# Kernel optimization log

Measured on AMD Instinct MI355X. Metric: run time of the kernel, lower is better.

## Reference

```python
import jax, jax.numpy as jnp
import numpy as np

B = 8
NUM_CLASSES = 80
STRIDES = (8, 16, 32, 64, 128)
HS = (96, 48, 24, 12, 6)
WS = (160, 80, 40, 20, 10)
IMG_H, IMG_W = 768, 1280
OCTAVE_SCALE = 4.0
LOC_THR = 0.01
SCORE_THR = 0.05
IOU_THR = 0.5
NMS_PRE = 1000
MAX_PER_IMG = 100
MAX_RATIO_ANCHOR = abs(float(np.log(1e-6)))        # anchor_coder wh_ratio_clip=1e-6
MAX_RATIO_BBOX = abs(float(np.log(16.0 / 1000.0)))  # bbox_coder default wh_ratio_clip
CLS_OFFSET = 4096.0  # > max image coord, separates classes for class-aware NMS


def setup_inputs():
    inp = {}
    k = 0
    for i, (h, w) in enumerate(zip(HS, WS)):
        for name, c in (("cls_score", NUM_CLASSES), ("bbox_pred", 4), ("shape_pred", 2), ("loc_pred", 1)):
            k += 1
            inp[f"{name}_{i}"] = jax.random.normal(jax.random.fold_in(jax.random.key(0), k), (B, c, h, w), dtype=jnp.float32)
    return inp


def _squares(h, w, stride):
    # mmdet square anchor generator: base size stride*octave_base_scale, ratio 1, center offset 0
    xs = jnp.arange(w, dtype=jnp.float32) * stride
    ys = jnp.arange(h, dtype=jnp.float32) * stride
    yy, xx = jnp.meshgrid(ys, xs, indexing="ij")
    half = 0.5 * OCTAVE_SCALE * stride
    return jnp.stack([xx - half, yy - half, xx + half, yy + half], -1).reshape(-1, 4)


def _delta2bbox(rois, deltas, max_ratio, max_shape=None):
    dx, dy = deltas[..., 0], deltas[..., 1]
    dw = jnp.clip(deltas[..., 2], -max_ratio, max_ratio)
    dh = jnp.clip(deltas[..., 3], -max_ratio, max_ratio)
    px = (rois[..., 0] + rois[..., 2]) * 0.5
    py = (rois[..., 1] + rois[..., 3]) * 0.5
    pw = rois[..., 2] - rois[..., 0]
    ph = rois[..., 3] - rois[..., 1]
    gx = px + pw * dx
    gy = py + ph * dy
    gw = pw * jnp.exp(dw)
    gh = ph * jnp.exp(dh)
    x1, y1 = gx - 0.5 * gw, gy - 0.5 * gh
    x2, y2 = gx + 0.5 * gw, gy + 0.5 * gh
    if max_shape is not None:
        x1 = jnp.clip(x1, 0.0, float(max_shape[1]))
        x2 = jnp.clip(x2, 0.0, float(max_shape[1]))
        y1 = jnp.clip(y1, 0.0, float(max_shape[0]))
        y2 = jnp.clip(y2, 0.0, float(max_shape[0]))
    return jnp.stack([x1, y1, x2, y2], -1)


def _level(cls, bbox, shp, loc, stride, h, w):
    b = cls.shape[0]
    # NOTE: double sigmoid is faithful to the original wrapper (it sigmoids twice)
    scores = jax.nn.sigmoid(jax.nn.sigmoid(jnp.transpose(cls, (0, 2, 3, 1)).reshape(b, -1, NUM_CLASSES)))
    mask = (jax.nn.sigmoid(loc) >= LOC_THR).astype(scores.dtype)
    mask = jnp.transpose(mask, (0, 2, 3, 1)).reshape(b, -1)  # num_anchors == 1
    scores = scores * mask[:, :, None]
    deltas = jnp.transpose(shp, (0, 2, 3, 1)).reshape(b, -1, 2)
    bdel = jnp.concatenate([jnp.zeros_like(deltas), deltas], axis=-1)  # [0,0,dw,dh]
    anchors = _delta2bbox(_squares(h, w, stride)[None], bdel, MAX_RATIO_ANCHOR)  # guided anchors
    bbox = jnp.transpose(bbox, (0, 2, 3, 1)).reshape(b, -1, 4)
    n = scores.shape[1]
    if n < NMS_PRE:  # pad_with_value
        pad = NMS_PRE - n
        scores = jnp.pad(scores, ((0, 0), (0, pad), (0, 0)))
        bbox = jnp.pad(bbox, ((0, 0), (0, pad), (0, 0)))
        anchors = jnp.pad(anchors, ((0, 0), (0, pad), (0, 0)))
    _, idx = jax.lax.top_k(scores.max(-1), NMS_PRE)
    scores = jnp.take_along_axis(scores, idx[:, :, None], axis=1)
    bbox = jnp.take_along_axis(bbox, idx[:, :, None], axis=1)
    anchors = jnp.take_along_axis(anchors, idx[:, :, None], axis=1)
    proposals = _delta2bbox(anchors, bbox, MAX_RATIO_BBOX, (IMG_H, IMG_W))
    return scores, proposals


def _iou_one_vs_all(box, boxes):
    lt = jnp.maximum(box[:2], boxes[:, :2])
    rb = jnp.minimum(box[2:], boxes[:, 2:])
    wh = jnp.clip(rb - lt, 0.0, None)
    inter = wh[:, 0] * wh[:, 1]
    a1 = (box[2] - box[0]) * (box[3] - box[1])
    a2 = (boxes[:, 2] - boxes[:, 0]) * (boxes[:, 3] - boxes[:, 1])
    return inter / (a1 + a2 - inter + 1e-6)


def _nms_single(scores, boxes):
    # class-aware greedy NMS (BatchedNMS semantics): scores [N,C], boxes [N,4]
    n, c = scores.shape
    s = jnp.where(scores > SCORE_THR, scores, 0.0).reshape(-1)  # [N*C]
    offs = (jnp.arange(c, dtype=boxes.dtype) * CLS_OFFSET)[None, :, None]
    cboxes = (boxes[:, None, :] + offs).reshape(-1, 4)  # class-offset boxes

    def step(sv, _):
        i = jnp.argmax(sv)
        sc = sv[i]
        keep = sc > 0.0
        iou = _iou_one_vs_all(cboxes[i], cboxes)
        sv = jnp.where(iou > IOU_THR, 0.0, sv)  # suppresses i itself too
        cls = jnp.where(keep, (i % c).astype(jnp.int32), -1)
        return sv, (boxes[i // c], sc, cls, keep)

    _, (ob, osc, ocls, okeep) = jax.lax.scan(step, s, None, length=MAX_PER_IMG)
    kf = okeep.astype(boxes.dtype)
    return okeep.sum().astype(jnp.int32), ob * kf[:, None], osc * kf, ocls


def _forward(tensors):
    mlvl_scores, mlvl_props = [], []
    for i in range(5):
        s, p = _level(tensors[4 * i], tensors[4 * i + 1], tensors[4 * i + 2], tensors[4 * i + 3],
                      STRIDES[i], HS[i], WS[i])
        mlvl_scores.append(s)
        mlvl_props.append(p)
    scores = jnp.concatenate(mlvl_scores, axis=1)   # [B, 5000, 80]
    props = jnp.concatenate(mlvl_props, axis=1)     # [B, 5000, 4]
    k = min(max(1000, NMS_PRE), scores.shape[1])
    _, idx = jax.lax.top_k(scores.max(-1), k)
    scores = jnp.take_along_axis(scores, idx[:, :, None], axis=1)
    props = jnp.take_along_axis(props, idx[:, :, None], axis=1)
    return jax.vmap(_nms_single)(scores, props)


def reference(cls_score_0, bbox_pred_0, shape_pred_0, loc_pred_0,
              cls_score_1, bbox_pred_1, shape_pred_1, loc_pred_1,
              cls_score_2, bbox_pred_2, shape_pred_2, loc_pred_2,
              cls_score_3, bbox_pred_3, shape_pred_3, loc_pred_3,
              cls_score_4, bbox_pred_4, shape_pred_4, loc_pred_4):
    tensors = [cls_score_0, bbox_pred_0, shape_pred_0, loc_pred_0,
               cls_score_1, bbox_pred_1, shape_pred_1, loc_pred_1,
               cls_score_2, bbox_pred_2, shape_pred_2, loc_pred_2,
               cls_score_3, bbox_pred_3, shape_pred_3, loc_pred_3,
               cls_score_4, bbox_pred_4, shape_pred_4, loc_pred_4]
    num_detected, proposals, out_scores, cls_id = _forward(tensors)
    return num_detected, proposals, out_scores, cls_id
```

## Files before the change

kernel.cpp:

```cpp
#include <hip/hip_runtime.h>
#include <stdint.h>

#define NCLS 80
#define BATCH 8
#define NA 20460
#define TOPK 1000
#define MAXPER 100
#define CAP 8
#define POOL 256
#define IMG_WF 1280.0f
#define IMG_HF 768.0f
#define CLS_OFF 4096.0f
#define MAX_RATIO_ANCHOR 13.815510557964274f
#define MAX_RATIO_BBOX   4.1351665567423557f

#define K2_HALF_UP (0.5 + 0x1p-25)

__constant__ int   c_lvoff[6]  = {0, 15360, 19200, 20160, 20400, 20460};
__constant__ int   c_lvoff4[6] = {0, 3840, 4800, 5040, 5100, 5115};
__constant__ int   c_lw[5]    = {160, 80, 40, 20, 10};
__constant__ int   c_lh[5]    = {96, 48, 24, 12, 6};
__constant__ float c_ls[5]    = {8.f, 16.f, 32.f, 64.f, 128.f};

struct InPtrs {
  const float* cls[5];
  const float* bbox[5];
  const float* shp[5];
  const float* loc[5];
};

__device__ __forceinline__ float sigf(float x) { return 1.0f / (1.0f + expf(-x)); }

__device__ __forceinline__ int wave_red_sum_i32(int v) {
  int t;
  t = __builtin_amdgcn_update_dpp(0, v, 0x111, 0xf, 0xf, false); v += t;
  t = __builtin_amdgcn_update_dpp(0, v, 0x112, 0xf, 0xf, false); v += t;
  t = __builtin_amdgcn_update_dpp(0, v, 0x114, 0xf, 0xf, false); v += t;
  t = __builtin_amdgcn_update_dpp(0, v, 0x118, 0xf, 0xf, false); v += t;
  t = __builtin_amdgcn_update_dpp(0, v, 0x142, 0xf, 0xf, false); v += t;
  t = __builtin_amdgcn_update_dpp(0, v, 0x143, 0xf, 0xf, false); v += t;
  return __builtin_amdgcn_readlane(v, 63);
}
__device__ __forceinline__ void wave_red_top2(unsigned m1, unsigned m2,
                                              unsigned& r1, unsigned& r2) {
#define T2STEP(ctrl) { \
    unsigned o1 = (unsigned)__builtin_amdgcn_update_dpp(0, (int)m1, ctrl, 0xf, 0xf, false); \
    unsigned o2 = (unsigned)__builtin_amdgcn_update_dpp(0, (int)m2, ctrl, 0xf, 0xf, false); \
    unsigned tm = min(m1, o1); \
    m1 = max(m1, o1); \
    m2 = max(tm, max(m2, o2)); }
  T2STEP(0x111) T2STEP(0x112) T2STEP(0x114) T2STEP(0x118) T2STEP(0x142) T2STEP(0x143)
#undef T2STEP
  r1 = (unsigned)__builtin_amdgcn_readlane((int)m1, 63);
  r2 = (unsigned)__builtin_amdgcn_readlane((int)m2, 63);
}

__global__ __launch_bounds__(256) void k_maxscore(InPtrs P, float* maxscore) {
  int gid = blockIdx.x * 256 + threadIdx.x;
  int p = gid >> 2;
  int h = gid & 3;
  if (p >= BATCH * (NA / 4)) return;
  int b = p / (NA / 4);
  int q = p - b * (NA / 4);
  int l = 0;
  while (q >= c_lvoff4[l + 1]) ++l;
  int hw = c_lh[l] * c_lw[l];
  int sp = (q - c_lvoff4[l]) * 4;
  const float4* cls = (const float4*)(P.cls[l] + (size_t)(b * NCLS + h * 20) * hw + sp);
  int s4 = hw >> 2;
  float4 m = cls[0];
  for (int c = 1; c < NCLS / 4; ++c) {
    float4 v = cls[(size_t)c * s4];
    m.x = fmaxf(m.x, v.x); m.y = fmaxf(m.y, v.y);
    m.z = fmaxf(m.z, v.z); m.w = fmaxf(m.w, v.w);
  }
  #pragma unroll
  for (int o = 1; o < 4; o <<= 1) {
    m.x = fmaxf(m.x, __shfl_xor(m.x, o, 64));
    m.y = fmaxf(m.y, __shfl_xor(m.y, o, 64));
    m.z = fmaxf(m.z, __shfl_xor(m.z, o, 64));
    m.w = fmaxf(m.w, __shfl_xor(m.w, o, 64));
  }
  if (h == 0) {
    float4 lo = *(const float4*)(P.loc[l] + (size_t)b * hw + sp);
    float4 r;
    r.x = (sigf(lo.x) >= 0.01f) ? sigf(sigf(m.x)) : 0.0f;
    r.y = (sigf(lo.y) >= 0.01f) ? sigf(sigf(m.y)) : 0.0f;
    r.z = (sigf(lo.z) >= 0.01f) ? sigf(sigf(m.z)) : 0.0f;
    r.w = (sigf(lo.w) >= 0.01f) ? sigf(sigf(m.w)) : 0.0f;
    ((float4*)maxscore)[(size_t)b * (NA / 4) + q] = r;
  }
}

__global__ __launch_bounds__(1024) void k_select(const float* maxscore, int* sel) {
  int b = blockIdx.x;
  const unsigned int* ms = (const unsigned int*)(maxscore + (size_t)b * NA);
  int tid = threadIdx.x;
  int wv = tid >> 6;
  int lane = tid & 63;
  __shared__ unsigned s_h[2048];
  __shared__ int s_wtot[16];
  __shared__ int s_res[2];
  __shared__ unsigned long long s_A[1024];
  __shared__ unsigned long long s_B[1024];

  unsigned w[20];
  #pragma unroll
  for (int k = 0; k < 5; ++k) {
    int q = tid * 5 + k;
    uint4 u = (q < NA / 4) ? ((const uint4*)ms)[q] : make_uint4(0u, 0u, 0u, 0u);
    w[k * 4 + 0] = u.x & 0x3FFFFFu;
    w[k * 4 + 1] = u.y & 0x3FFFFFu;
    w[k * 4 + 2] = u.z & 0x3FFFFFu;
    w[k * 4 + 3] = u.w & 0x3FFFFFu;
  }
  int lim = NA - tid * 20;
  lim = (lim < 0) ? 0 : ((lim > 20) ? 20 : lim);

  s_h[tid] = 0u; s_h[tid + 1024] = 0u;
  __syncthreads();

  auto scanFind = [&](int target) {
    int b0 = 2047 - 2 * tid;
    int h0 = (int)s_h[b0];
    int h1 = (int)s_h[b0 - 1];
    int pair = h0 + h1;
    int incl = pair;
    #pragma unroll
    for (int o = 1; o < 64; o <<= 1) {
      int uu = __shfl_up(incl, o, 64);
      if (lane >= o) incl += uu;
    }
    if (lane == 63) s_wtot[wv] = incl;
    __syncthreads();
    int woff = 0;
    #pragma unroll
    for (int ww = 0; ww < 16; ++ww) woff += (ww < wv) ? s_wtot[ww] : 0;
    int excl = woff + incl - pair;
    if (excl < target && excl + h0 >= target) { s_res[0] = b0; s_res[1] = excl; }
    int e1 = excl + h0;
    if (e1 < target && e1 + h1 >= target) { s_res[0] = b0 - 1; s_res[1] = e1; }
    __syncthreads();
  };

  #pragma unroll
  for (int k = 0; k < 20; ++k) atomicAdd(&s_h[w[k] >> 11], 1u);
  __syncthreads();
  scanFind(TOPK);
  int B1 = s_res[0];
  int NGT1 = s_res[1];

  s_h[tid] = 0u; s_h[tid + 1024] = 0u;
  __syncthreads();
  #pragma unroll
  for (int k = 0; k < 20; ++k)
    if ((int)(w[k] >> 11) == B1) atomicAdd(&s_h[w[k] & 0x7FFu], 1u);
  __syncthreads();
  scanFind(TOPK - NGT1);
  unsigned V = ((unsigned)B1 << 11) | (unsigned)s_res[0];

  if (tid < 1024 - TOPK) s_A[TOPK + tid] = 0ull;

  int cgt = 0;
  #pragma unroll
  for (int k = 0; k < 20; ++k) cgt += (w[k] > V) ? 1 : 0;
  {
    int incl = cgt;
    #pragma unroll
    for (int o = 1; o < 64; o <<= 1) {
      int uu = __shfl_up(incl, o, 64);
      if (lane >= o) incl += uu;
    }
    if (lane == 63) s_wtot[wv] = incl;
    __syncthreads();
    int woff = 0, tot = 0;
    #pragma unroll
    for (int ww = 0; ww < 16; ++ww) { tot += s_wtot[ww]; woff += (ww < wv) ? s_wtot[ww] : 0; }
    int pos = woff + incl - cgt;
    #pragma unroll
    for (int k = 0; k < 20; ++k) {
      if (w[k] > V) {
        int i = tid * 20 + k;
        s_A[pos++] = ((unsigned long long)w[k] << 32) |
                     (unsigned long long)(0xFFFFFFFFu - (unsigned)i);
      }
    }
    int ngt = tot;
    int need = TOPK - ngt;
    __syncthreads();

    int ceq = 0;
    #pragma unroll
    for (int k = 0; k < 20; ++k) if (k < lim && w[k] == V) ++ceq;
    int incl2 = ceq;
    #pragma unroll
    for (int o = 1; o < 64; o <<= 1) {
      int uu = __shfl_up(incl2, o, 64);
      if (lane >= o) incl2 += uu;
    }
    if (lane == 63) s_wtot[wv] = incl2;
    __syncthreads();
    int woff2 = 0;
    #pragma unroll
    for (int ww = 0; ww < 16; ++ww) woff2 += (ww < wv) ? s_wtot[ww] : 0;
    int r = woff2 + incl2 - ceq;
    #pragma unroll
    for (int k = 0; k < 20; ++k) {
      if (k < lim && w[k] == V) {
        if (r < need) {
          int i = tid * 20 + k;
          s_A[ngt + r] = ((unsigned long long)V << 32) |
                         (unsigned long long)(0xFFFFFFFFu - (unsigned)i);
        }
        ++r;
      }
    }
  }
  __syncthreads();

  unsigned long long key = s_A[tid];
  int tog = 0;
  for (unsigned k = 2; k <= 1024; k <<= 1) {
    for (unsigned j = k >> 1; j > 0; j >>= 1) {
      unsigned long long other;
      if (j >= 64) {
        unsigned long long* cur = tog ? s_A : s_B;
        cur[tid] = key;
        __syncthreads();
        other = cur[tid ^ (int)j];
        tog ^= 1;
      } else {
        other = __shfl_xor(key, (int)j, 64);
      }
      bool takeMax = (((tid & (int)k) == 0) == ((tid & (int)j) == 0));
      unsigned long long mx = (key > other) ? key : other;
      unsigned long long mn = (key > other) ? other : key;
      key = takeMax ? mx : mn;
    }
  }
  if (tid < TOPK) {
    sel[b * TOPK + tid] = (int)(0xFFFFFFFFu - (unsigned)(key & 0xFFFFFFFFull));
  }
}

__global__ __launch_bounds__(256) void k_gather(InPtrs P, const int* sel, float* boxes, float* sv) {
  int wvi = threadIdx.x >> 6;
  int lane = threadIdx.x & 63;
  int wid = blockIdx.x * 4 + wvi;
  int b = wid / TOPK;
  int r = wid - b * TOPK;
  __shared__ float s_sc[4][NCLS];

  int a = sel[b * TOPK + r];
  int l = 0;
  while (a >= c_lvoff[l + 1]) ++l;
  int within = a - c_lvoff[l];
  int W = c_lw[l], H = c_lh[l];
  int y = within / W, x = within - y * W;
  int hw = H * W;
  int sp = within;
  float stride = c_ls[l];
  float px = (float)x * stride;
  float py = (float)y * stride;
  float pw = 4.0f * stride;

  const float* shp = P.shp[l];
  float dws = shp[(b * 2 + 0) * hw + sp];
  float dhs = shp[(b * 2 + 1) * hw + sp];
  dws = fminf(fmaxf(dws, -MAX_RATIO_ANCHOR), MAX_RATIO_ANCHOR);
  dhs = fminf(fmaxf(dhs, -MAX_RATIO_ANCHOR), MAX_RATIO_ANCHOR);
  float gw = pw * expf(dws);
  float gh = pw * expf(dhs);
  float ax1 = px - 0.5f * gw, ax2 = px + 0.5f * gw;
  float ay1 = py - 0.5f * gh, ay2 = py + 0.5f * gh;

  const float* bb = P.bbox[l];
  float dx = bb[(b * 4 + 0) * hw + sp];
  float dy = bb[(b * 4 + 1) * hw + sp];
  float dw = bb[(b * 4 + 2) * hw + sp];
  float dh = bb[(b * 4 + 3) * hw + sp];
  dw = fminf(fmaxf(dw, -MAX_RATIO_BBOX), MAX_RATIO_BBOX);
  dh = fminf(fmaxf(dh, -MAX_RATIO_BBOX), MAX_RATIO_BBOX);
  float px2 = (ax1 + ax2) * 0.5f, py2 = (ay1 + ay2) * 0.5f;
  float pw2 = ax2 - ax1, ph2 = ay2 - ay1;
  float gx = px2 + pw2 * dx, gy = py2 + ph2 * dy;
  float gw2 = pw2 * expf(dw), gh2 = ph2 * expf(dh);
  float x1 = fminf(fmaxf(gx - 0.5f * gw2, 0.0f), IMG_WF);
  float x2 = fminf(fmaxf(gx + 0.5f * gw2, 0.0f), IMG_WF);
  float y1 = fminf(fmaxf(gy - 0.5f * gh2, 0.0f), IMG_HF);
  float y2 = fminf(fmaxf(gy + 0.5f * gh2, 0.0f), IMG_HF);
  if (lane == 0) {
    float4 st; st.x = x1; st.y = y1; st.z = x2; st.w = y2;
    ((float4*)boxes)[b * TOPK + r] = st;
  }

  const float* cls = P.cls[l];
  float sl = sigf(P.loc[l][b * hw + sp]);
  bool mask = (sl >= 0.01f);
  int base = (b * NCLS) * hw + sp;
  for (int c = lane; c < NCLS; c += 64) {
    float vv = 0.0f;
    if (mask) {
      float s2 = sigf(sigf(cls[base + c * hw]));
      vv = (s2 > 0.05f) ? s2 : 0.0f;
    }
    s_sc[wvi][c] = vv;
  }
  __syncthreads();
  int t = threadIdx.x;
  if (t < NCLS) {
    int r0 = blockIdx.x * 4 - b * TOPK;
    float4 o; o.x = s_sc[0][t]; o.y = s_sc[1][t]; o.z = s_sc[2][t]; o.w = s_sc[3][t];
    *(float4*)(sv + ((size_t)(b * NCLS + t) * TOPK + r0)) = o;
  }
}

__global__ __launch_bounds__(256) void k_nms(const float* boxes, const float* sv,
                                             float* keptScore, int* keptRow, int* kc,
                                             const int* flags, const int* gbits, int cap) {
  int bc = blockIdx.x;
  if (flags && flags[bc] == 0) return;
  int b = bc / NCLS;
  int c = bc - b * NCLS;
  int tid = threadIdx.x;
  int wv = tid >> 6, lane = tid & 63;

  unsigned Glow = 0u;
  if (gbits) Glow = ((unsigned)gbits[b]) & 0x3FFFFFu;

  __shared__ float4 s_box[TOPK];
  __shared__ float  s_ard[TOPK];
  __shared__ unsigned long long s_p2[2][4];

  float x1[4], y1[4], x2[4], y2[4], ar[4];
  unsigned key[4];
  float off = (float)c * CLS_OFF;
  const float* svc = sv + (size_t)(b * NCLS + c) * TOPK;
  #pragma unroll
  for (int j = 0; j < 4; ++j) {
    int row = j * 256 + tid;
    if (row < TOPK) {
      float4 bo = ((const float4*)boxes)[b * TOPK + row];
      float a = bo.x + off, d = bo.y + off, e = bo.z + off, f = bo.w + off;
      x1[j] = a; y1[j] = d; x2[j] = e; y2[j] = f;
      ar[j] = (e - a) * (f - d);
      unsigned bits = __float_as_uint(svc[row]);
      key[j] = ((bits & 0x3FFFFFu) << 10) | (1023u - (unsigned)row);
      float sden = ar[j] + 1e-6f;
      bool deg = !((double)ar[j] > (double)sden * K2_HALF_UP);
      float4 sb; sb.x = a; sb.y = d; sb.z = e; sb.w = f;
      s_box[row] = sb;
      s_ard[row] = __uint_as_float(__float_as_uint(ar[j]) | (deg ? 0x80000000u : 0u));
    } else {
      x1[j] = y1[j] = x2[j] = y2[j] = ar[j] = 0.0f;
      key[j] = 0u;
    }
  }
  __syncthreads();

  int kept = 0;
  bool sticky = false;
  float* ks = keptScore + (size_t)(b * NCLS + c) * MAXPER;
  int*   kr = keptRow   + (size_t)(b * NCLS + c) * MAXPER;

  for (int round = 0; round < cap; ++round) {
    int par = round & 1;
    unsigned hi1 = max(key[0], key[1]), lo1 = min(key[0], key[1]);
    unsigned hi2 = max(key[2], key[3]), lo2 = min(key[2], key[3]);
    unsigned m1 = max(hi1, hi2);
    unsigned m2 = max(min(hi1, hi2), max(lo1, lo2));
    unsigned w1, w2;
    wave_red_top2(m1, m2, w1, w2);
    if (lane == 0) s_p2[par][wv] = ((unsigned long long)w1 << 32) | w2;
    __syncthreads();
    unsigned k0 = 0u, k1 = 0u;
    #pragma unroll
    for (int w = 0; w < 4; ++w) {
      unsigned long long pp = s_p2[par][w];
      unsigned p1 = (unsigned)(pp >> 32), p2 = (unsigned)pp;
      unsigned tm = min(k0, p1);
      k0 = max(k0, p1);
      k1 = max(tm, max(k1, p2));
    }
    if (k0 < 1024u) break;
    if ((k0 >> 10) < Glow) break;
    int brow1 = 1023 - (int)(k0 & 1023u);
    float bs1 = __uint_as_float(0x3F000000u | (k0 >> 10));
    float4 bb1 = s_box[brow1];
    unsigned au1 = __float_as_uint(s_ard[brow1]);
    bool deg1 = (au1 >> 31) != 0u;
    float ba1 = __uint_as_float(au1 & 0x7FFFFFFFu);
    if (tid == 0) { ks[kept] = bs1; kr[kept] = brow1; }
    kept++;
    if (deg1) { sticky = true; break; }
    if (kept >= cap) break;
    bool live2 = (k1 >= 1024u) && ((k1 >> 10) >= Glow);
    if (!live2) break;
    bool do2 = false, deg2 = false;
    float4 bb2; float ba2 = 0.0f;
    {
      int brow2 = 1023 - (int)(k1 & 1023u);
      float bs2 = __uint_as_float(0x3F000000u | (k1 >> 10));
      bb2 = s_box[brow2];
      unsigned au2 = __float_as_uint(s_ard[brow2]);
      deg2 = (au2 >> 31) != 0u;
      ba2 = __uint_as_float(au2 & 0x7FFFFFFFu);
      float ltx = fmaxf(bb1.x, bb2.x), rbx = fminf(bb1.z, bb2.z);
      float lty = fmaxf(bb1.y, bb2.y), rby = fminf(bb1.w, bb2.w);
      float w_ = fmaxf(rbx - ltx, 0.0f), h_ = fmaxf(rby - lty, 0.0f);
      float inter = w_ * h_;
      float denom = ((ba1 + ba2) - inter) + 1e-6f;
      if (!((double)inter > (double)denom * K2_HALF_UP)) {
        do2 = true;
        if (tid == 0) { ks[kept] = bs2; kr[kept] = brow2; }
        kept++;
      }
    }
    if (do2 && deg2) { sticky = true; break; }
    #pragma unroll
    for (int j = 0; j < 4; ++j) {
      {
        float ltx = fmaxf(bb1.x, x1[j]), rbx = fminf(bb1.z, x2[j]);
        float lty = fmaxf(bb1.y, y1[j]), rby = fminf(bb1.w, y2[j]);
        float w_ = fmaxf(rbx - ltx, 0.0f), h_ = fmaxf(rby - lty, 0.0f);
        float inter = w_ * h_;
        float denom = ((ba1 + ar[j]) - inter) + 1e-6f;
        if ((double)inter > (double)denom * K2_HALF_UP) key[j] = 0u;
      }
      if (do2) {
        float ltx = fmaxf(bb2.x, x1[j]), rbx = fminf(bb2.z, x2[j]);
        float lty = fmaxf(bb2.y, y1[j]), rby = fminf(bb2.w, y2[j]);
        float w_ = fmaxf(rbx - ltx, 0.0f), h_ = fmaxf(rby - lty, 0.0f);
        float inter = w_ * h_;
        float denom = ((ba2 + ar[j]) - inter) + 1e-6f;
        if ((double)inter > (double)denom * K2_HALF_UP) key[j] = 0u;
      }
    }
    if (kept >= cap) break;
  }
  if (tid == 0) kc[b * NCLS + c] = sticky ? -kept : kept;
}

__global__ __launch_bounds__(256) void k_cut(const float* keptScore, const int* kc,
                                             int* flags, int* gbits) {
  int b = blockIdx.x;
  int tid = threadIdx.x;
  int wv = tid >> 6, lane = tid & 63;
  __shared__ int s_abs[NCLS];
  __shared__ int s_neg[NCLS];
  __shared__ unsigned s_h[2048];
  __shared__ int s_wtot[4];
  __shared__ int s_res[2];
  __shared__ int s_tot[4];

  if (tid < NCLS) {
    int v = kc[b * NCLS + tid];
    s_abs[tid] = (v < 0) ? -v : v;
    s_neg[tid] = (v < 0) ? 1 : 0;
  }
  #pragma unroll
  for (int j = 0; j < 8; ++j) s_h[tid * 8 + j] = 0u;
  __syncthreads();

  unsigned vv[3] = {0u, 0u, 0u};
  #pragma unroll
  for (int t = 0; t < 3; ++t) {
    int e = tid + t * 256;
    if (e < NCLS * CAP) {
      int c = e / CAP, k = e - c * CAP;
      if (k < s_abs[c])
        vv[t] = __float_as_uint(keptScore[(size_t)b * NCLS * MAXPER + c * MAXPER + k])
                & 0x3FFFFFu;
    }
  }
  int live = ((vv[0] != 0u) ? 1 : 0) + ((vv[1] != 0u) ? 1 : 0) + ((vv[2] != 0u) ? 1 : 0);
  live = wave_red_sum_i32(live);
  if (lane == 0) s_tot[wv] = live;
  #pragma unroll
  for (int t = 0; t < 3; ++t) if (vv[t]) atomicAdd(&s_h[vv[t] >> 11], 1u);
  __syncthreads();
  int T = s_tot[0] + s_tot[1] + s_tot[2] + s_tot[3];

  auto scanFind = [&](int target) {
    int base = 2047 - 8 * tid;
    int h[8]; int loc = 0;
    #pragma unroll
    for (int j = 0; j < 8; ++j) { h[j] = (int)s_h[base - j]; loc += h[j]; }
    int incl = loc;
    #pragma unroll
    for (int o = 1; o < 64; o <<= 1) {
      int uu = __shfl_up(incl, o, 64);
      if (lane >= o) incl += uu;
    }
    if (lane == 63) s_wtot[wv] = incl;
    __syncthreads();
    int woff = 0;
    #pragma unroll
    for (int ww = 0; ww < 4; ++ww) woff += (ww < wv) ? s_wtot[ww] : 0;
    int e = woff + incl - loc;
    #pragma unroll
    for (int j = 0; j < 8; ++j) {
      if (e < target && e + h[j] >= target) { s_res[0] = base - j; s_res[1] = e; }
      e += h[j];
    }
    __syncthreads();
  };

  unsigned G = 0u;
  if (T >= MAXPER) {
    scanFind(MAXPER);
    int B1 = s_res[0], NGT1 = s_res[1];
    #pragma unroll
    for (int j = 0; j < 8; ++j) s_h[tid * 8 + j] = 0u;
    __syncthreads();
    #pragma unroll
    for (int t = 0; t < 3; ++t)
      if (vv[t] && (int)(vv[t] >> 11) == B1) atomicAdd(&s_h[vv[t] & 0x7FFu], 1u);
    __syncthreads();
    scanFind(MAXPER - NGT1);
    G = 0x3F000000u | ((unsigned)B1 << 11) | (unsigned)s_res[0];
  }
  if (tid == 0) gbits[b] = (int)G;
  if (tid < NCLS) {
    int f = 0;
    if (s_abs[tid] == CAP && !s_neg[tid]) {
      unsigned slast = __float_as_uint(
          keptScore[(size_t)b * NCLS * MAXPER + tid * MAXPER + (CAP - 1)]);
      if (slast >= G) f = 1;
    }
    flags[b * NCLS + tid] = f;
  }
}

__global__ __launch_bounds__(256) void k_merge(const float* boxes, const float* keptScore,
                                               const int* keptRow, const int* kc, float* out) {
  int b = blockIdx.x;
  int tid = threadIdx.x;
  int wv = tid >> 6, lane = tid & 63;
  __shared__ int s_kc[NCLS];
  __shared__ unsigned s_h[2048];
  __shared__ int s_wtot[4];
  __shared__ int s_res[2];
  __shared__ int s_tot[4];
  __shared__ int s_pos;
  __shared__ int s_sticky;
  __shared__ int s_navail;
  __shared__ unsigned long long s_pool[POOL];
  __shared__ unsigned long long s_sorted[POOL];

  for (int c = tid; c < NCLS; c += 256) s_kc[c] = kc[b * NCLS + c];
  if (tid == 0) { s_pos = 0; s_sticky = 0x7FFFFFFF; s_navail = 0; }
  for (int i = tid; i < POOL; i += 256) { s_pool[i] = 0ull; s_sorted[i] = 0ull; }
  #pragma unroll
  for (int j = 0; j < 8; ++j) s_h[tid * 8 + j] = 0u;
  __syncthreads();

  unsigned sc[32];
  #pragma unroll
  for (int s = 0; s < 32; ++s) {
    int i = tid + s * 256;
    unsigned vvv = 0u;
    if (i < NCLS * MAXPER) {
      int c = i / MAXPER, k = i - c * MAXPER;
      int kcv = s_kc[c];
      int ka = (kcv < 0) ? -kcv : kcv;
      if (k < ka)
        vvv = __float_as_uint(keptScore[(size_t)b * NCLS * MAXPER + i]) & 0x3FFFFFu;
    }
    sc[s] = vvv;
  }
  int live = 0;
  #pragma unroll
  for (int s = 0; s < 32; ++s) live += (sc[s] != 0u) ? 1 : 0;
  live = wave_red_sum_i32(live);
  if (lane == 0) s_tot[wv] = live;
  #pragma unroll
  for (int s = 0; s < 32; ++s) if (sc[s]) atomicAdd(&s_h[sc[s] >> 11], 1u);
  __syncthreads();
  int T = s_tot[0] + s_tot[1] + s_tot[2] + s_tot[3];

  auto scanFind = [&](int target) {
    int base = 2047 - 8 * tid;
    int h[8]; int loc = 0;
    #pragma unroll
    for (int j = 0; j < 8; ++j) { h[j] = (int)s_h[base - j]; loc += h[j]; }
    int incl = loc;
    #pragma unroll
    for (int o = 1; o < 64; o <<= 1) {
      int uu = __shfl_up(incl, o, 64);
      if (lane >= o) incl += uu;
    }
    if (lane == 63) s_wtot[wv] = incl;
    __syncthreads();
    int woff = 0;
    #pragma unroll
    for (int ww = 0; ww < 4; ++ww) woff += (ww < wv) ? s_wtot[ww] : 0;
    int e = woff + incl - loc;
    #pragma unroll
    for (int j = 0; j < 8; ++j) {
      if (e < target && e + h[j] >= target) { s_res[0] = base - j; s_res[1] = e; }
      e += h[j];
    }
    __syncthreads();
  };

  unsigned V = 1u;
  if (T > MAXPER) {
    scanFind(MAXPER);
    int B1 = s_res[0], NGT1 = s_res[1];
    #pragma unroll
    for (int j = 0; j < 8; ++j) s_h[tid * 8 + j] = 0u;
    __syncthreads();
    #pragma unroll
    for (int s = 0; s < 32; ++s)
      if (sc[s] && (int)(sc[s] >> 11) == B1) atomicAdd(&s_h[sc[s] & 0x7FFu], 1u);
    __syncthreads();
    scanFind(MAXPER - NGT1);
    V = ((unsigned)B1 << 11) | (unsigned)s_res[0];
  }

  #pragma unroll
  for (int s = 0; s < 32; ++s) {
    if (sc[s] >= V && sc[s] != 0u) {
      int i = tid + s * 256;
      int c = i / MAXPER, k = i - c * MAXPER;
      int kcv = s_kc[c];
      int ka = (kcv < 0) ? -kcv : kcv;
      unsigned st = (kcv < 0 && k == ka - 1) ? 1u : 0u;
      unsigned row = (unsigned)keptRow[(size_t)b * NCLS * MAXPER + i];
      unsigned flat = row * 80u + (unsigned)c;
      int p = atomicAdd(&s_pos, 1);
      if (p < POOL)
        s_pool[p] = ((unsigned long long)(0x3F000000u | sc[s]) << 32) |
                    (unsigned long long)(0x7FFFFFFFu - ((flat << 1) | st));
    }
  }
  __syncthreads();

  if (tid < POOL) {
    unsigned long long mykey = s_pool[tid];
    if (mykey != 0ull) {
      int rank = 0;
      #pragma unroll 8
      for (int s = 0; s < POOL; ++s) rank += (s_pool[s] > mykey) ? 1 : 0;
      s_sorted[rank] = mykey;
    }
  }
  __syncthreads();

  if (tid < MAXPER) {
    unsigned long long key = s_sorted[tid];
    if (key != 0ull) {
      atomicAdd(&s_navail, 1);
      if ((((unsigned)key) & 1u) == 0u) atomicMin(&s_sticky, tid);
    }
  }
  __syncthreads();
  int navail = s_navail;
  int p = s_sticky;
  int n = (p < navail) ? MAXPER : navail;

  if (tid == 0) out[b] = (float)n;
  const int OB = BATCH;
  const int OP = OB + BATCH * MAXPER * 4;
  const int OS = OP + BATCH * MAXPER;
  if (tid < MAXPER) {
    int k = tid;
    float bx0 = 0.f, bx1 = 0.f, bx2 = 0.f, bx3 = 0.f, scf = 0.f, cf = -1.0f;
    if (k < n) {
      int idx = (k > p) ? p : k;
      unsigned long long key = s_sorted[idx];
      unsigned flat = (0x7FFFFFFFu - (unsigned)key) >> 1;
      unsigned cls = flat % 80u;
      unsigned row = flat / 80u;
      float4 bo = ((const float4*)boxes)[b * TOPK + row];
      bx0 = bo.x; bx1 = bo.y; bx2 = bo.z; bx3 = bo.w;
      scf = __uint_as_float((unsigned)(key >> 32));
      cf = (float)cls;
    }
    float* po = out + OB + (size_t)(b * MAXPER + k) * 4;
    po[0] = bx0; po[1] = bx1; po[2] = bx2; po[3] = bx3;
    out[OP + b * MAXPER + k] = scf;
    out[OS + b * MAXPER + k] = cf;
  }
}

extern "C" void kernel_launch(void* const* d_in, const int* in_sizes, int n_in,
                              void* d_out, int out_size, void* d_ws, size_t ws_size,
                              hipStream_t stream) {
  InPtrs P;
  for (int l = 0; l < 5; ++l) {
    P.cls[l]  = (const float*)d_in[4 * l + 0];
    P.bbox[l] = (const float*)d_in[4 * l + 1];
    P.shp[l]  = (const float*)d_in[4 * l + 2];
    P.loc[l]  = (const float*)d_in[4 * l + 3];
  }
  float* maxscore  = (float*)d_ws;
  int*   sel       = (int*)(maxscore + BATCH * NA);
  float* boxes     = (float*)(sel + BATCH * TOPK);
  float* sv        = boxes + BATCH * TOPK * 4;
  float* keptScore = sv + BATCH * NCLS * TOPK;
  int*   keptRow   = (int*)(keptScore + BATCH * NCLS * MAXPER);
  int*   kc        = keptRow + BATCH * NCLS * MAXPER;
  int*   flags     = kc + BATCH * NCLS;
  int*   gbits     = flags + BATCH * NCLS;
  float* out = (float*)d_out;

  k_maxscore<<<(BATCH * (NA / 4) * 4 + 255) / 256, 256, 0, stream>>>(P, maxscore);
  k_select<<<BATCH, 1024, 0, stream>>>(maxscore, sel);
  k_gather<<<BATCH * TOPK / 4, 256, 0, stream>>>(P, sel, boxes, sv);
  k_nms<<<BATCH * NCLS, 256, 0, stream>>>(boxes, sv, keptScore, keptRow, kc,
                                          (const int*)nullptr, (const int*)nullptr, CAP);
  k_cut<<<BATCH, 256, 0, stream>>>(keptScore, kc, flags, gbits);
  k_nms<<<BATCH * NCLS, 256, 0, stream>>>(boxes, sv, keptScore, keptRow, kc,
                                          flags, gbits, MAXPER);
  k_merge<<<BATCH, 256, 0, stream>>>(boxes, keptScore, keptRow, kc, out);
}
```

Measured before the change: 194.7 us.

## Widen k_merge to 1024 threads and compact the candidate pool with a prefix scan

k_merge now runs 1024 threads per image instead of 256. Each thread holds 8 candidate scores instead of 32, and the histogram scan covers 2 bins per thread across 16 waves. The shared atomic counter that placed survivors into the pool is replaced by a wave and block prefix sum, which gives each thread its write offsets directly. The aim is to cut the latency of this single-block-per-image tail kernel, at the cost of more barriers and cross-wave reductions. Only 8 blocks launch, so any effect on total time is limited.

```diff
diff --git a/kernel.cpp b/kernel.cpp
--- a/kernel.cpp
+++ b/kernel.cpp
@@ -532,33 +532,30 @@
   }
 }
 
-__global__ __launch_bounds__(256) void k_merge(const float* boxes, const float* keptScore,
-                                               const int* keptRow, const int* kc, float* out) {
+__global__ __launch_bounds__(1024) void k_merge(const float* boxes, const float* keptScore,
+                                                const int* keptRow, const int* kc, float* out) {
   int b = blockIdx.x;
   int tid = threadIdx.x;
   int wv = tid >> 6, lane = tid & 63;
   __shared__ int s_kc[NCLS];
   __shared__ unsigned s_h[2048];
-  __shared__ int s_wtot[4];
+  __shared__ int s_wtot[16];
   __shared__ int s_res[2];
-  __shared__ int s_tot[4];
-  __shared__ int s_pos;
   __shared__ int s_sticky;
   __shared__ int s_navail;
   __shared__ unsigned long long s_pool[POOL];
   __shared__ unsigned long long s_sorted[POOL];
 
-  for (int c = tid; c < NCLS; c += 256) s_kc[c] = kc[b * NCLS + c];
-  if (tid == 0) { s_pos = 0; s_sticky = 0x7FFFFFFF; s_navail = 0; }
-  for (int i = tid; i < POOL; i += 256) { s_pool[i] = 0ull; s_sorted[i] = 0ull; }
-  #pragma unroll
-  for (int j = 0; j < 8; ++j) s_h[tid * 8 + j] = 0u;
-  __syncthreads();
-
-  unsigned sc[32];
-  #pragma unroll
-  for (int s = 0; s < 32; ++s) {
-    int i = tid + s * 256;
+  if (tid < NCLS) s_kc[tid] = kc[b * NCLS + tid];
+  if (tid == 0) { s_sticky = 0x7FFFFFFF; s_navail = 0; }
+  if (tid < POOL) { s_pool[tid] = 0ull; s_sorted[tid] = 0ull; }
+  s_h[tid] = 0u; s_h[tid + 1024] = 0u;
+  __syncthreads();
+
+  unsigned sc[8];
+  #pragma unroll
+  for (int s = 0; s < 8; ++s) {
+    int i = tid + s * 1024;
     unsigned vvv = 0u;
     if (i < NCLS * MAXPER) {
       int c = i / MAXPER, k = i - c * MAXPER;
@@ -571,20 +568,22 @@
   }
   int live = 0;
   #pragma unroll
-  for (int s = 0; s < 32; ++s) live += (sc[s] != 0u) ? 1 : 0;
+  for (int s = 0; s < 8; ++s) live += (sc[s] != 0u) ? 1 : 0;
   live = wave_red_sum_i32(live);
-  if (lane == 0) s_tot[wv] = live;
-  #pragma unroll
-  for (int s = 0; s < 32; ++s) if (sc[s]) atomicAdd(&s_h[sc[s] >> 11], 1u);
-  __syncthreads();
-  int T = s_tot[0] + s_tot[1] + s_tot[2] + s_tot[3];
+  if (lane == 0) s_wtot[wv] = live;
+  #pragma unroll
+  for (int s = 0; s < 8; ++s) if (sc[s]) atomicAdd(&s_h[sc[s] >> 11], 1u);
+  __syncthreads();
+  int T = 0;
+  #pragma unroll
+  for (int ww = 0; ww < 16; ++ww) T += s_wtot[ww];
 
   auto scanFind = [&](int target) {
-    int base = 2047 - 8 * tid;
-    int h[8]; int loc = 0;
-    #pragma unroll
-    for (int j = 0; j < 8; ++j) { h[j] = (int)s_h[base - j]; loc += h[j]; }
-    int incl = loc;
+    int b0 = 2047 - 2 * tid;
+    int h0 = (int)s_h[b0];
+    int h1 = (int)s_h[b0 - 1];
+    int pair = h0 + h1;
+    int incl = pair;
     #pragma unroll
     for (int o = 1; o < 64; o <<= 1) {
       int uu = __shfl_up(incl, o, 64);
@@ -594,13 +593,11 @@
     __syncthreads();
     int woff = 0;
     #pragma unroll
-    for (int ww = 0; ww < 4; ++ww) woff += (ww < wv) ? s_wtot[ww] : 0;
-    int e = woff + incl - loc;
-    #pragma unroll
-    for (int j = 0; j < 8; ++j) {
-      if (e < target && e + h[j] >= target) { s_res[0] = base - j; s_res[1] = e; }
-      e += h[j];
-    }
+    for (int ww = 0; ww < 16; ++ww) woff += (ww < wv) ? s_wtot[ww] : 0;
+    int excl = woff + incl - pair;
+    if (excl < target && excl + h0 >= target) { s_res[0] = b0; s_res[1] = excl; }
+    int e1 = excl + h0;
+    if (e1 < target && e1 + h1 >= target) { s_res[0] = b0 - 1; s_res[1] = e1; }
     __syncthreads();
   };
 
@@ -608,31 +605,47 @@
   if (T > MAXPER) {
     scanFind(MAXPER);
     int B1 = s_res[0], NGT1 = s_res[1];
-    #pragma unroll
-    for (int j = 0; j < 8; ++j) s_h[tid * 8 + j] = 0u;
-    __syncthreads();
-    #pragma unroll
-    for (int s = 0; s < 32; ++s)
+    s_h[tid] = 0u; s_h[tid + 1024] = 0u;
+    __syncthreads();
+    #pragma unroll
+    for (int s = 0; s < 8; ++s)
       if (sc[s] && (int)(sc[s] >> 11) == B1) atomicAdd(&s_h[sc[s] & 0x7FFu], 1u);
     __syncthreads();
     scanFind(MAXPER - NGT1);
     V = ((unsigned)B1 << 11) | (unsigned)s_res[0];
   }
 
-  #pragma unroll
-  for (int s = 0; s < 32; ++s) {
-    if (sc[s] >= V && sc[s] != 0u) {
-      int i = tid + s * 256;
-      int c = i / MAXPER, k = i - c * MAXPER;
-      int kcv = s_kc[c];
-      int ka = (kcv < 0) ? -kcv : kcv;
-      unsigned st = (kcv < 0 && k == ka - 1) ? 1u : 0u;
-      unsigned row = (unsigned)keptRow[(size_t)b * NCLS * MAXPER + i];
-      unsigned flat = row * 80u + (unsigned)c;
-      int p = atomicAdd(&s_pos, 1);
-      if (p < POOL)
-        s_pool[p] = ((unsigned long long)(0x3F000000u | sc[s]) << 32) |
-                    (unsigned long long)(0x7FFFFFFFu - ((flat << 1) | st));
+  {
+    int cg = 0;
+    #pragma unroll
+    for (int s = 0; s < 8; ++s) cg += (sc[s] >= V) ? 1 : 0;
+    int incl = cg;
+    #pragma unroll
+    for (int o = 1; o < 64; o <<= 1) {
+      int uu = __shfl_up(incl, o, 64);
+      if (lane >= o) incl += uu;
+    }
+    if (lane == 63) s_wtot[wv] = incl;
+    __syncthreads();
+    int woff = 0;
+    #pragma unroll
+    for (int ww = 0; ww < 16; ++ww) woff += (ww < wv) ? s_wtot[ww] : 0;
+    int pos = woff + incl - cg;
+    #pragma unroll
+    for (int s = 0; s < 8; ++s) {
+      if (sc[s] >= V) {
+        int i = tid + s * 1024;
+        int c = i / MAXPER, k = i - c * MAXPER;
+        int kcv = s_kc[c];
+        int ka = (kcv < 0) ? -kcv : kcv;
+        unsigned st = (kcv < 0 && k == ka - 1) ? 1u : 0u;
+        unsigned row = (unsigned)keptRow[(size_t)b * NCLS * MAXPER + i];
+        unsigned flat = row * 80u + (unsigned)c;
+        if (pos < POOL)
+          s_pool[pos] = ((unsigned long long)(0x3F000000u | sc[s]) << 32) |
+                        (unsigned long long)(0x7FFFFFFFu - ((flat << 1) | st));
+        ++pos;
+      }
     }
   }
   __syncthreads();
@@ -714,5 +727,5 @@
   k_cut<<<BATCH, 256, 0, stream>>>(keptScore, kc, flags, gbits);
   k_nms<<<BATCH * NCLS, 256, 0, stream>>>(boxes, sv, keptScore, keptRow, kc,
                                           flags, gbits, MAXPER);
-  k_merge<<<BATCH, 256, 0, stream>>>(boxes, keptScore, keptRow, kc, out);
-}
+  k_merge<<<BATCH, 1024, 0, stream>>>(boxes, keptScore, keptRow, kc, out);
+}
```

Result: faster. 187.2 us (-3.9%).
